# Kernel optimization log

Measured on AMD Instinct MI355X. Metric: run time of the kernel, lower is better.

## Reference

```python
import jax, jax.numpy as jnp
import numpy as np

B, T, N, H, E, K, HOR, OD = 64, 12, 1024, 64, 16, 3, 12, 1
DIN = 1  # input_dim
EPS = 1e-12


def setup_inputs() -> dict:
    key = jax.random.key(0)
    ks = jax.random.split(key, 8)
    s = 0.02
    return {
        "source": jax.random.normal(ks[0], (B, T, N, DIN), jnp.float32),
        "node_emb": jax.random.normal(ks[1], (N, E), jnp.float32),
        "time_emb": jax.random.normal(ks[2], (T, E), jnp.float32),
        "gate_wp": jax.random.normal(ks[3], (E, K, DIN + H, 2 * H), jnp.float32) * s,
        "gate_bp": jax.random.normal(ks[4], (E, 2 * H), jnp.float32) * s,
        "gate_lng": jnp.ones((E,), jnp.float32),
        "gate_lnb": jnp.zeros((E,), jnp.float32),
        "upd_wp": jax.random.normal(ks[5], (E, K, DIN + H, H), jnp.float32) * s,
        "upd_bp": jax.random.normal(ks[6], (E, H), jnp.float32) * s,
        "upd_lng": jnp.ones((E,), jnp.float32),
        "upd_lnb": jnp.zeros((E,), jnp.float32),
        "out_lng": jnp.ones((H,), jnp.float32),
        "out_lnb": jnp.zeros((H,), jnp.float32),
        "conv_w": jax.random.normal(ks[7], (HOR * OD, H), jnp.float32) * s,
        "conv_b": jnp.zeros((HOR * OD,), jnp.float32),
    }


def _ln(x, g, b):
    m = x.mean(-1, keepdims=True)
    v = x.var(-1, keepdims=True)
    return (x - m) / jnp.sqrt(v + EPS) * g + b


def _dagcn(x, node_emb, t_emb, wp, bp, lng, lnb):
    # x: [B, N, C]; node_emb: [N, E]; t_emb: [E] (one timestep)
    e = _ln(node_emb + t_emb[None, :], lng, lnb)          # [N, E] (dropout off in eval)
    sup = jax.nn.softmax(e @ e.T, axis=1)                  # [N, N]
    sl = [jnp.eye(N, dtype=x.dtype), sup]
    for _ in range(2, K):
        sl.append(2.0 * sup @ sl[-1] - sl[-2])             # Chebyshev recursion
    S = jnp.stack(sl, axis=0)                              # [K, N, N]
    w = jnp.einsum('nd,dkio->nkio', e, wp)                 # per-node weights
    bias = e @ bp                                          # [N, O]
    xg = jnp.einsum('knm,bmc->bnkc', S, x)                 # graph conv
    return jnp.einsum('bnki,nkio->bno', xg, w) + bias


def reference(source, node_emb, time_emb, gate_wp, gate_bp, gate_lng, gate_lnb,
              upd_wp, upd_bp, upd_lng, upd_lnb, out_lng, out_lnb, conv_w, conv_b):
    def step(state, xs):
        x_t, te = xs                                        # [B,N,DIN], [E]
        zr = jax.nn.sigmoid(_dagcn(jnp.concatenate([x_t, state], -1),
                                   node_emb, te, gate_wp, gate_bp, gate_lng, gate_lnb))
        z, r = zr[..., :H], zr[..., H:]
        hc = jnp.tanh(_dagcn(jnp.concatenate([x_t, z * state], -1),
                             node_emb, te, upd_wp, upd_bp, upd_lng, upd_lnb))
        h = r * state + (1.0 - r) * hc
        return h, None

    xs = jnp.swapaxes(source, 0, 1)                        # [T,B,N,DIN]
    h0 = jnp.zeros((B, N, H), source.dtype)
    h, _ = jax.lax.scan(step, h0, (xs, time_emb))          # last hidden state [B,N,H]
    y = _ln(h, out_lng, out_lnb)                           # out_dropout off in eval
    out = jnp.einsum('bnh,oh->bon', y, conv_w) + conv_b[None, :, None]  # end_conv
    return out.reshape(B, HOR, OD, N).transpose(0, 1, 3, 2)  # [B,horizon,N,output_dim]
```

## Files before the change

### kernel.cpp

```cpp
#include <hip/hip_runtime.h>
#include <math.h>

namespace {
constexpr int B_ = 64, T_ = 12, N_ = 1024, H_ = 64, E_ = 16;
constexpr int C_  = 65;
constexpr int BC_ = B_ * C_;
constexpr int OG_ = 128;
constexpr int OU_ = 64;
constexpr float EPS_ = 1e-12f;
constexpr int NP_ = 4224;
constexpr int KP_ = 224;
constexpr int COLG_ = OG_ * KP_;
constexpr int COLU_ = OU_ * KP_;
constexpr int NE_ = N_ * E_;
}

typedef unsigned short u16;
typedef unsigned int u32;
using f16x8 = __attribute__((ext_vector_type(8))) _Float16;
using f16x4 = __attribute__((ext_vector_type(4))) _Float16;
using f32x4 = __attribute__((ext_vector_type(4))) float;

__device__ __forceinline__ u32 div65(u32 x) { return (x * 16135u) >> 20; }

__device__ __forceinline__ void gl_lds16(const void* g, void* l, int lane) {
#if __has_builtin(__builtin_amdgcn_global_load_lds)
  __builtin_amdgcn_global_load_lds((const __attribute__((address_space(1))) u32*)g,
                                   (__attribute__((address_space(3))) u32*)l, 16, 0, 0);
#else
  *(uint4*)((char*)l + lane * 16) = *(const uint4*)g;
#endif
}

__device__ __forceinline__ void wprep_body(const float* __restrict__ wp, int NO,
                                           _Float16* __restrict__ wpC, int k, int tid) {
  if (tid >= NO) return;
  f16x8 lo = {}, hi = {};
  if (k < 195) {
    const u32 seg = div65((u32)k);
    const u32 ii = k - seg * 65;
#pragma unroll
    for (int d = 0; d < 8; d++)
      lo[d] = (_Float16)wp[(((size_t)d * 3 + seg) * 65 + ii) * NO + tid];
#pragma unroll
    for (int d = 0; d < 8; d++)
      hi[d] = (_Float16)wp[(((size_t)(d + 8) * 3 + seg) * 65 + ii) * NO + tid];
  }
  _Float16* dst = &wpC[((size_t)tid * KP_ + k) * 16];
  *(f16x8*)dst = lo;
  *(f16x8*)(dst + 8) = hi;
}

__device__ __forceinline__ void sup_body(const float* __restrict__ eT,
                                         _Float16* __restrict__ s16,
                                         int n, int tid, float* red) {
  float en[E_];
#pragma unroll
  for (int d = 0; d < E_; d++) en[d] = eT[d * N_ + n];
  float lg[4];
  float mx = -3.4e38f;
#pragma unroll
  for (int j = 0; j < 4; j++) {
    int m = tid + 256 * j;
    float s = 0.f;
#pragma unroll
    for (int d = 0; d < E_; d++) s = fmaf(en[d], eT[d * N_ + m], s);
    lg[j] = s;
    mx = fmaxf(mx, s);
  }
  red[tid] = mx; __syncthreads();
  for (int off = 128; off > 0; off >>= 1) {
    if (tid < off) red[tid] = fmaxf(red[tid], red[tid + off]);
    __syncthreads();
  }
  mx = red[0]; __syncthreads();
  float sum = 0.f;
#pragma unroll
  for (int j = 0; j < 4; j++) { lg[j] = __expf(lg[j] - mx); sum += lg[j]; }
  red[tid] = sum; __syncthreads();
  for (int off = 128; off > 0; off >>= 1) {
    if (tid < off) red[tid] += red[tid + off];
    __syncthreads();
  }
  float inv = 1.0f / red[0];
#pragma unroll
  for (int j = 0; j < 4; j++)
    s16[(size_t)n * N_ + tid + 256 * j] = (_Float16)(lg[j] * inv);
}

__device__ __forceinline__ void wgen_body(const float* __restrict__ e,
                                          const _Float16* __restrict__ wpC, int COLS,
                                          _Float16* __restrict__ Wt,
                                          int xb, int yb, int tid, float (*es)[16]) {
  const int col0 = xb * 1024 + tid * 4;
  const int n0 = yb * 64;
#pragma unroll
  for (int q = 0; q < 4; q++) {
    int idx = tid + q * 256;
    es[idx >> 4][idx & 15] = e[(size_t)n0 * 16 + idx];
  }
  __syncthreads();
  float wc[4][16];
#pragma unroll
  for (int cc = 0; cc < 4; cc++) {
    f16x8 a = *(const f16x8*)&wpC[(size_t)(col0 + cc) * 16];
    f16x8 b = *(const f16x8*)&wpC[(size_t)(col0 + cc) * 16 + 8];
#pragma unroll
    for (int d = 0; d < 8; d++) { wc[cc][d] = (float)a[d]; wc[cc][8 + d] = (float)b[d]; }
  }
  for (int nn = 0; nn < 64; nn++) {
    float acc[4] = {};
#pragma unroll
    for (int d = 0; d < 16; d++) {
      float ev = es[nn][d];
#pragma unroll
      for (int cc = 0; cc < 4; cc++) acc[cc] = fmaf(ev, wc[cc][d], acc[cc]);
    }
    f16x4 pv;
#pragma unroll
    for (int cc = 0; cc < 4; cc++) pv[cc] = (_Float16)acc[cc];
    *(f16x4*)&Wt[(size_t)(n0 + nn) * COLS + col0] = pv;
  }
}

__device__ __forceinline__ void gemm_body(
    const _Float16* __restrict__ A, const _Float16* __restrict__ Bt,
    _Float16* __restrict__ yt, _Float16* xg, int segoff, int combine,
    int bx, int by, int tid, _Float16* As, _Float16* Bs) {
  const int wave = tid >> 6, lane = tid & 63;
  const int m0 = by * 128, c0 = bx * 64;
  const int lrow = lane >> 3;
  const int lchunk = lane & 7;
  const int fm = lane & 15, fq = lane >> 4;
  f32x4 acc[2][4] = {};
  for (int ks = 0; ks < 16; ks++) {
    const int kp = ks * 64;
#pragma unroll
    for (int q = 0; q < 4; q++) {
      const int seg = wave * 4 + q;
      const int row = seg * 8 + lrow;
      const int sw = lchunk ^ (row & 7);
      gl_lds16(A + (size_t)(m0 + row) * 1024 + kp + sw * 8, &As[seg * 8 * 64], lane);
    }
#pragma unroll
    for (int q = 0; q < 2; q++) {
      const int seg = wave * 2 + q;
      const int row = seg * 8 + lrow;
      const int sw = lchunk ^ (row & 7);
      gl_lds16(Bt + (size_t)(c0 + row) * 1024 + kp + sw * 8, &Bs[seg * 8 * 64], lane);
    }
    __syncthreads();
#pragma unroll
    for (int kk = 0; kk < 2; kk++) {
      f16x8 af[2], bfr[4];
      const int g = kk * 4 + fq;
#pragma unroll
      for (int mt = 0; mt < 2; mt++) {
        const int row = wave * 32 + mt * 16 + fm;
        af[mt] = *(const f16x8*)&As[row * 64 + (g ^ (row & 7)) * 8];
      }
#pragma unroll
      for (int nt = 0; nt < 4; nt++) {
        const int row = nt * 16 + fm;
        bfr[nt] = *(const f16x8*)&Bs[row * 64 + (g ^ (row & 7)) * 8];
      }
#pragma unroll
      for (int mt = 0; mt < 2; mt++)
#pragma unroll
        for (int nt = 0; nt < 4; nt++)
          acc[mt][nt] = __builtin_amdgcn_mfma_f32_16x16x32_f16(af[mt], bfr[nt], acc[mt][nt], 0, 0, 0);
    }
    __syncthreads();
  }
  const int q4 = fq * 4;
#pragma unroll
  for (int nt = 0; nt < 4; nt++) {
    const int col = c0 + nt * 16 + fm;
    if (col >= BC_) continue;
    const u32 bq = div65((u32)col), cq = (u32)col - bq * 65;
#pragma unroll
    for (int mt = 0; mt < 2; mt++) {
      const int row = m0 + wave * 32 + mt * 16 + q4;
      const f32x4 v = acc[mt][nt];
      if (yt) {
        f16x4 pv;
#pragma unroll
        for (int j = 0; j < 4; j++) pv[j] = (_Float16)v[j];
        *(f16x4*)&yt[(size_t)col * 1024 + row] = pv;
      }
#pragma unroll
      for (int j = 0; j < 4; j++) {
        size_t base = ((size_t)(row + j) * 64 + bq) * KP_;
        float vv = v[j];
        if (combine) vv = 2.f * vv - (float)xg[base + cq];
        xg[base + segoff + cq] = (_Float16)vv;
      }
    }
  }
}

__global__ __launch_bounds__(256) void k_pre0(
    const float* __restrict__ gate_wp, const float* __restrict__ upd_wp,
    _Float16* __restrict__ wpCg, _Float16* __restrict__ wpCu,
    const float* __restrict__ node_emb, const float* __restrict__ time_emb,
    const float* __restrict__ g_lng, const float* __restrict__ g_lnb,
    const float* __restrict__ u_lng, const float* __restrict__ u_lnb,
    float* __restrict__ eg_all, float* __restrict__ egT_all,
    float* __restrict__ eu_all, float* __restrict__ euT_all) {
  const int bid = blockIdx.x, tid = threadIdx.x;
  if (bid < KP_)     { wprep_body(gate_wp, OG_, wpCg, bid, tid); return; }
  if (bid < 2 * KP_) { wprep_body(upd_wp,  OU_, wpCu, bid - KP_, tid); return; }
  const int idx = bid - 2 * KP_;
  const int t = idx >> 2;
  const int n = (idx & 3) * 256 + tid;
  float v[E_];
  float m = 0.f;
#pragma unroll
  for (int d = 0; d < E_; d++) { v[d] = node_emb[n * E_ + d] + time_emb[t * E_ + d]; m += v[d]; }
  m *= (1.0f / E_);
  float var = 0.f;
#pragma unroll
  for (int d = 0; d < E_; d++) { float x = v[d] - m; var += x * x; }
  var *= (1.0f / E_);
  float rs = rsqrtf(var + EPS_);
#pragma unroll
  for (int d = 0; d < E_; d++) {
    float nv = (v[d] - m) * rs;
    float g = nv * g_lng[d] + g_lnb[d];
    float u = nv * u_lng[d] + u_lnb[d];
    eg_all[(size_t)t * NE_ + n * E_ + d] = g;
    egT_all[(size_t)t * NE_ + d * N_ + n] = g;
    eu_all[(size_t)t * NE_ + n * E_ + d] = u;
    euT_all[(size_t)t * NE_ + d * N_ + n] = u;
  }
}

__global__ __launch_bounds__(256) void k_pro(
    const float* __restrict__ egT0, const float* __restrict__ euT0,
    const float* __restrict__ src,
    _Float16* __restrict__ supG, _Float16* __restrict__ supU0,
    _Float16* __restrict__ Xt, _Float16* __restrict__ xg) {
  __shared__ float red[256];
  const int bid = blockIdx.x, tid = threadIdx.x;
  if (bid < 1024) { sup_body(egT0, supG, bid, tid, red); return; }
  if (bid < 2048) { sup_body(euT0, supU0, bid - 1024, tid, red); return; }
  const int idx = bid - 2048;
  const int b = idx & 63, m0 = (idx >> 6) * 64;
  for (int q = 0; q < 17; q++) {
    int i = tid + q * 256;
    if (i < 64 * 65) {
      int c = i >> 6, m = i & 63;
      float xv = (c == 0) ? src[((size_t)b * T_) * N_ + m0 + m] : 0.f;
      Xt[((size_t)(b * C_ + c)) * 1024 + m0 + m] = (_Float16)xv;
      u32 mm = div65((u32)i), cc = (u32)i - mm * 65;
      float xv2 = (cc == 0) ? src[((size_t)b * T_) * N_ + m0 + mm] : 0.f;
      xg[((size_t)(m0 + mm) * 64 + b) * KP_ + cc] = (_Float16)xv2;
    }
  }
#pragma unroll
  for (int q = 0; q < 8; q++) {
    int i = tid + q * 256;
    int mm = i >> 5, kk = 192 + (i & 31);
    xg[((size_t)(m0 + mm) * 64 + b) * KP_ + kk] = (_Float16)0.f;
  }
}

__global__ __launch_bounds__(256) void k_tr(const _Float16* __restrict__ xg,
                                            _Float16* __restrict__ Xt) {
  __shared__ _Float16 tile[64][66];
  const int b = blockIdx.x & 63, m0 = (blockIdx.x >> 6) * 64;
  const int tid = threadIdx.x;
  {
    const int m = tid >> 2, c4 = tid & 3;
    const _Float16* rp = &xg[((size_t)(m0 + m) * 64 + b) * KP_ + c4 * 16];
    f16x8 v0 = *(const f16x8*)rp;
    f16x8 v1 = *(const f16x8*)(rp + 8);
#pragma unroll
    for (int i = 0; i < 8; i++) {
      tile[m][c4 * 16 + i] = v0[i];
      tile[m][c4 * 16 + 8 + i] = v1[i];
    }
    if (c4 == 0) tile[m][64] = rp[64];
  }
  __syncthreads();
  {
    const int m = tid & 63, cg = tid >> 6;
    for (int cc = cg; cc < 65; cc += 4)
      Xt[((size_t)(b * C_ + cc)) * 1024 + m0 + m] = tile[m][cc];
  }
}

__global__ __launch_bounds__(256) void k_g1(
    const _Float16* __restrict__ supG, const _Float16* __restrict__ Xt,
    _Float16* __restrict__ y1t, _Float16* xg,
    const float* __restrict__ eg_t, const _Float16* __restrict__ wpCg,
    _Float16* __restrict__ WtG) {
  __shared__ __align__(16) _Float16 smem[12288];
  const int bid = blockIdx.x, tid = threadIdx.x;
  if (bid < 528) {
    gemm_body(supG, Xt, y1t, xg, 65, 0, bid % 66, bid / 66, tid, smem, smem + 8192);
  } else {
    const int w = bid - 528;
    wgen_body(eg_t, wpCg, COLG_, WtG, w % 28, w / 28, tid, (float(*)[16])smem);
  }
}

__global__ __launch_bounds__(256) void k_g2(
    const _Float16* __restrict__ supG, const _Float16* __restrict__ y1t,
    _Float16* xg) {
  __shared__ __align__(16) _Float16 smem[12288];
  gemm_body(supG, y1t, nullptr, xg, 130, 1, blockIdx.x % 66, blockIdx.x / 66,
            threadIdx.x, smem, smem + 8192);
}

__global__ __launch_bounds__(256) void k_g3(
    const _Float16* __restrict__ supU, const _Float16* __restrict__ Xt,
    _Float16* __restrict__ y1t, _Float16* xg,
    const float* __restrict__ eu_t, const _Float16* __restrict__ wpCu,
    _Float16* __restrict__ WtU) {
  __shared__ __align__(16) _Float16 smem[12288];
  const int bid = blockIdx.x, tid = threadIdx.x;
  if (bid < 528) {
    gemm_body(supU, Xt, y1t, xg, 65, 0, bid % 66, bid / 66, tid, smem, smem + 8192);
  } else {
    const int w = bid - 528;
    wgen_body(eu_t, wpCu, COLU_, WtU, w % 14, w / 14, tid, (float(*)[16])smem);
  }
}

__global__ __launch_bounds__(256) void k_g4(
    const _Float16* __restrict__ supU, const _Float16* __restrict__ y1t,
    _Float16* xg,
    const float* __restrict__ egT_nx, const float* __restrict__ euT_nx,
    _Float16* __restrict__ supG, _Float16* __restrict__ supU_nx, int dosup) {
  __shared__ __align__(16) _Float16 smem[12288];
  const int bid = blockIdx.x, tid = threadIdx.x;
  if (bid < 528) {
    gemm_body(supU, y1t, nullptr, xg, 130, 1, bid % 66, bid / 66, tid, smem, smem + 8192);
  } else if (dosup) {
    if (bid < 1552) sup_body(egT_nx, supG, bid - 528, tid, (float*)smem);
    else            sup_body(euT_nx, supU_nx, bid - 1552, tid, (float*)smem);
  }
}

__global__ __launch_bounds__(256) void k_cg(
    const float* __restrict__ eg, const _Float16* XG,
    const _Float16* __restrict__ Wt, const float* __restrict__ bp,
    const _Float16* __restrict__ h16, const float* __restrict__ src, int t,
    _Float16* __restrict__ r16, _Float16* xgo) {
  const int n = blockIdx.x;
  const int tid = threadIdx.x;
  const int wave = tid >> 6, lane = tid & 63;
  const int fm = lane & 15, fq = lane >> 4;
  const int wm = wave >> 1, wn = wave & 1;
  __shared__ float es[16];
  __shared__ float bias_s[128];
  __shared__ _Float16 zs[64][72];
  __shared__ _Float16 rs[64][72];
  if (tid < 16) es[tid] = eg[n * 16 + tid];
  __syncthreads();
  if (tid < 128) {
    float bv = 0.f;
#pragma unroll
    for (int d = 0; d < 16; d++) bv = fmaf(es[d], bp[d * OG_ + tid], bv);
    bias_s[tid] = bv;
  }
  const _Float16* Ab = XG + (size_t)n * 64 * KP_;
  const _Float16* Bb = Wt + (size_t)n * OG_ * KP_;
  f16x8 af[2][2], bf[2][4];
#pragma unroll
  for (int mt = 0; mt < 2; mt++)
    af[0][mt] = *(const f16x8*)&Ab[(wm * 32 + mt * 16 + fm) * KP_ + fq * 8];
#pragma unroll
  for (int nt = 0; nt < 4; nt++)
    bf[0][nt] = *(const f16x8*)&Bb[(wn * 64 + nt * 16 + fm) * KP_ + fq * 8];
  f32x4 acc[2][4] = {};
#pragma unroll
  for (int kk = 0; kk < 7; kk++) {
    const int cur = kk & 1;
    if (kk < 6) {
      const int ko = (kk + 1) * 32 + fq * 8;
#pragma unroll
      for (int mt = 0; mt < 2; mt++)
        af[cur ^ 1][mt] = *(const f16x8*)&Ab[(wm * 32 + mt * 16 + fm) * KP_ + ko];
#pragma unroll
      for (int nt = 0; nt < 4; nt++)
        bf[cur ^ 1][nt] = *(const f16x8*)&Bb[(wn * 64 + nt * 16 + fm) * KP_ + ko];
    }
#pragma unroll
    for (int mt = 0; mt < 2; mt++)
#pragma unroll
      for (int nt = 0; nt < 4; nt++)
        acc[mt][nt] = __builtin_amdgcn_mfma_f32_16x16x32_f16(af[cur][mt], bf[cur][nt], acc[mt][nt], 0, 0, 0);
  }
  __syncthreads();
#pragma unroll
  for (int nt = 0; nt < 4; nt++) {
    const int o = wn * 64 + nt * 16 + fm;
    const float bias = bias_s[o];
#pragma unroll
    for (int mt = 0; mt < 2; mt++) {
      const f32x4 v = acc[mt][nt];
#pragma unroll
      for (int j = 0; j < 4; j++) {
        const int b = wm * 32 + mt * 16 + fq * 4 + j;
        float s = 1.0f / (1.0f + __expf(-(v[j] + bias)));
        if (wn == 0) zs[b][o] = (_Float16)s;
        else         rs[b][o - H_] = (_Float16)s;
      }
    }
  }
  __syncthreads();
  {
    const int b = tid >> 2, q = tid & 3;
    const _Float16* hp = &h16[((size_t)b * N_ + n) * H_ + q * 16];
    _Float16* xp = &xgo[((size_t)n * 64 + b) * KP_ + 1 + q * 16];
    _Float16* rp = &r16[((size_t)b * N_ + n) * H_ + q * 16];
    f16x8 r0, r1;
#pragma unroll
    for (int i = 0; i < 8; i++) {
      r0[i] = rs[b][q * 16 + i];
      r1[i] = rs[b][q * 16 + 8 + i];
    }
    *(f16x8*)rp = r0;
    *(f16x8*)(rp + 8) = r1;
    f16x8 h0 = *(const f16x8*)hp;
    f16x8 h1 = *(const f16x8*)(hp + 8);
    f16x8 x0, x1;
#pragma unroll
    for (int i = 0; i < 8; i++) {
      x0[i] = (_Float16)((float)zs[b][q * 16 + i] * (float)h0[i]);
      x1[i] = (_Float16)((float)zs[b][q * 16 + 8 + i] * (float)h1[i]);
    }
    *(f16x8*)xp = x0;
    *(f16x8*)(xp + 8) = x1;
    if (tid < 64) {
      float sv = src[((size_t)tid * T_ + t) * N_ + n];
      xgo[((size_t)n * 64 + tid) * KP_] = (_Float16)sv;
    }
  }
}

__global__ __launch_bounds__(256) void k_cu(
    const float* __restrict__ eu, const _Float16* XG,
    const _Float16* __restrict__ Wt, const float* __restrict__ bp,
    const _Float16* __restrict__ r16, const float* __restrict__ src,
    int t, int donext,
    _Float16* __restrict__ h16, _Float16* xgo) {
  const int n = blockIdx.x;
  const int tid = threadIdx.x;
  const int wave = tid >> 6, lane = tid & 63;
  const int fm = lane & 15, fq = lane >> 4;
  __shared__ float es[16];
  __shared__ float bias_s[64];
  __shared__ _Float16 hs[64][72];
  __shared__ _Float16 rs[64][72];
  if (tid < 16) es[tid] = eu[n * 16 + tid];
  __syncthreads();
  if (tid < 64) {
    float bv = 0.f;
#pragma unroll
    for (int d = 0; d < 16; d++) bv = fmaf(es[d], bp[d * OU_ + tid], bv);
    bias_s[tid] = bv;
  }
  {
    const int b = tid >> 2, q = tid & 3;
    const _Float16* hp = &h16[((size_t)b * N_ + n) * H_ + q * 16];
    const _Float16* rp = &r16[((size_t)b * N_ + n) * H_ + q * 16];
    f16x8 h0 = *(const f16x8*)hp;
    f16x8 h1 = *(const f16x8*)(hp + 8);
    f16x8 r0 = *(const f16x8*)rp;
    f16x8 r1 = *(const f16x8*)(rp + 8);
#pragma unroll
    for (int i = 0; i < 8; i++) {
      hs[b][q * 16 + i] = h0[i];
      hs[b][q * 16 + 8 + i] = h1[i];
      rs[b][q * 16 + i] = r0[i];
      rs[b][q * 16 + 8 + i] = r1[i];
    }
  }
  __syncthreads();
  const _Float16* Ab = XG + (size_t)n * 64 * KP_;
  const _Float16* Bb = Wt + (size_t)n * OU_ * KP_;
  f16x8 af[2], bf[2][4];
  af[0] = *(const f16x8*)&Ab[(wave * 16 + fm) * KP_ + fq * 8];
#pragma unroll
  for (int nt = 0; nt < 4; nt++)
    bf[0][nt] = *(const f16x8*)&Bb[(nt * 16 + fm) * KP_ + fq * 8];
  f32x4 acc[4] = {};
#pragma unroll
  for (int kk = 0; kk < 7; kk++) {
    const int cur = kk & 1;
    if (kk < 6) {
      const int ko = (kk + 1) * 32 + fq * 8;
      af[cur ^ 1] = *(const f16x8*)&Ab[(wave * 16 + fm) * KP_ + ko];
#pragma unroll
      for (int nt = 0; nt < 4; nt++)
        bf[cur ^ 1][nt] = *(const f16x8*)&Bb[(nt * 16 + fm) * KP_ + ko];
    }
#pragma unroll
    for (int nt = 0; nt < 4; nt++)
      acc[nt] = __builtin_amdgcn_mfma_f32_16x16x32_f16(af[cur], bf[cur][nt], acc[nt], 0, 0, 0);
  }
#pragma unroll
  for (int nt = 0; nt < 4; nt++) {
    const int o = nt * 16 + fm;
    const float bias = bias_s[o];
    const f32x4 v = acc[nt];
#pragma unroll
    for (int j = 0; j < 4; j++) {
      const int b = wave * 16 + fq * 4 + j;
      float hc = tanhf(v[j] + bias);
      float rv = (float)rs[b][o];
      float hv = (float)hs[b][o];
      hs[b][o] = (_Float16)(rv * hv + (1.0f - rv) * hc);
    }
  }
  __syncthreads();
  {
    const int b = tid >> 2, q = tid & 3;
    _Float16* hp = &h16[((size_t)b * N_ + n) * H_ + q * 16];
    f16x8 h0, h1;
#pragma unroll
    for (int i = 0; i < 8; i++) {
      h0[i] = hs[b][q * 16 + i];
      h1[i] = hs[b][q * 16 + 8 + i];
    }
    *(f16x8*)hp = h0;
    *(f16x8*)(hp + 8) = h1;
    if (donext) {
      _Float16* xp = &xgo[((size_t)n * 64 + b) * KP_ + 1 + q * 16];
      *(f16x8*)xp = h0;
      *(f16x8*)(xp + 8) = h1;
      if (tid < 64) {
        float sv = src[((size_t)tid * T_ + (t + 1)) * N_ + n];
        xgo[((size_t)n * 64 + tid) * KP_] = (_Float16)sv;
      }
    }
  }
}

__global__ __launch_bounds__(256) void k_final(const _Float16* __restrict__ h16,
                                               const float* __restrict__ out_lng,
                                               const float* __restrict__ out_lnb,
                                               const float* __restrict__ conv_w,
                                               const float* __restrict__ conv_b,
                                               float* __restrict__ out) {
  const int b = blockIdx.x >> 2;
  const int n = (blockIdx.x & 3) * 256 + threadIdx.x;
  __shared__ float cw[12][64];
  __shared__ float cb[12];
  __shared__ float lgs[64], lbs[64];
  for (int idx = threadIdx.x; idx < 12 * 64; idx += 256) cw[idx >> 6][idx & 63] = conv_w[idx];
  if (threadIdx.x < 12) cb[threadIdx.x] = conv_b[threadIdx.x];
  if (threadIdx.x < 64) { lgs[threadIdx.x] = out_lng[threadIdx.x]; lbs[threadIdx.x] = out_lnb[threadIdx.x]; }
  __syncthreads();
  const _Float16* hp = &h16[((size_t)b * N_ + n) * H_];
  float hv[64];
  float mean = 0.f;
#pragma unroll
  for (int i8 = 0; i8 < 8; i8++) {
    f16x8 v = *(const f16x8*)&hp[i8 * 8];
#pragma unroll
    for (int j = 0; j < 8; j++) { hv[i8 * 8 + j] = (float)v[j]; mean += hv[i8 * 8 + j]; }
  }
  mean *= (1.0f / H_);
  float var = 0.f;
#pragma unroll
  for (int i = 0; i < 64; i++) { float d = hv[i] - mean; var += d * d; }
  var *= (1.0f / H_);
  const float rs = rsqrtf(var + EPS_);
  float y[64];
#pragma unroll
  for (int i = 0; i < 64; i++)
    y[i] = (hv[i] - mean) * rs * lgs[i] + lbs[i];
#pragma unroll
  for (int o = 0; o < 12; o++) {
    float acc = cb[o];
#pragma unroll
    for (int i = 0; i < 64; i++) acc = fmaf(y[i], cw[o][i], acc);
    out[((size_t)b * 12 + o) * N_ + n] = acc;
  }
}

extern "C" void kernel_launch(void* const* d_in, const int* in_sizes, int n_in,
                              void* d_out, int out_size, void* d_ws, size_t ws_size,
                              hipStream_t stream) {
  const float* src      = (const float*)d_in[0];
  const float* node_emb = (const float*)d_in[1];
  const float* time_emb = (const float*)d_in[2];
  const float* gate_wp  = (const float*)d_in[3];
  const float* gate_bp  = (const float*)d_in[4];
  const float* gate_lng = (const float*)d_in[5];
  const float* gate_lnb = (const float*)d_in[6];
  const float* upd_wp   = (const float*)d_in[7];
  const float* upd_bp   = (const float*)d_in[8];
  const float* upd_lng  = (const float*)d_in[9];
  const float* upd_lnb  = (const float*)d_in[10];
  const float* out_lng  = (const float*)d_in[11];
  const float* out_lnb  = (const float*)d_in[12];
  const float* conv_w   = (const float*)d_in[13];
  const float* conv_b   = (const float*)d_in[14];
  float* out = (float*)d_out;

  constexpr size_t SZ_H16 = (size_t)B_ * N_ * H_ / 2;
  constexpr size_t SZ_R   = SZ_H16;
  constexpr size_t SZ_T   = (size_t)NP_ * 1024 / 2;
  constexpr size_t SZ_XG  = (size_t)N_ * 64 * KP_ / 2;
  constexpr size_t SZ_WT  = (size_t)N_ * OG_ * KP_ / 2;
  constexpr size_t SZ_WCG = (size_t)COLG_ * 16 / 2;
  constexpr size_t SZ_WCU = (size_t)COLU_ * 16 / 2;
  constexpr size_t SZ_S   = (size_t)N_ * N_ / 2;

  float* ws = (float*)d_ws;
  size_t off = 0;
  float* h16F   = ws + off; off += SZ_H16;
  float* r16F   = ws + off; off += SZ_R;
  float* XtF    = ws + off; off += SZ_T;
  float* y1tF   = ws + off; off += SZ_T;
  float* xgF    = ws + off; off += SZ_XG;
  float* WtF    = ws + off; off += SZ_WT;
  float* wcgF   = ws + off; off += SZ_WCG;
  float* wcuF   = ws + off; off += SZ_WCU;
  float* supGF  = ws + off; off += SZ_S;
  float* supUF  = ws + off; off += 2 * SZ_S;
  float* eg_all  = ws + off; off += (size_t)T_ * NE_;
  float* egT_all = ws + off; off += (size_t)T_ * NE_;
  float* eu_all  = ws + off; off += (size_t)T_ * NE_;
  float* euT_all = ws + off; off += (size_t)T_ * NE_;
  if (ws_size < off * sizeof(float)) return;

  _Float16* h16  = (_Float16*)h16F;
  _Float16* r16  = (_Float16*)r16F;
  _Float16* Xt   = (_Float16*)XtF;
  _Float16* y1t  = (_Float16*)y1tF;
  _Float16* xg   = (_Float16*)xgF;
  _Float16* WtG  = (_Float16*)WtF;
  _Float16* WtU  = (_Float16*)WtF;
  _Float16* wpCg = (_Float16*)wcgF;
  _Float16* wpCu = (_Float16*)wcuF;
  _Float16* supG = (_Float16*)supGF;
  _Float16* supU = (_Float16*)supUF;

  hipMemsetAsync(h16, 0, SZ_H16 * sizeof(float), stream);
  k_pre0<<<2 * KP_ + 48, 256, 0, stream>>>(gate_wp, upd_wp, wpCg, wpCu,
                                           node_emb, time_emb,
                                           gate_lng, gate_lnb, upd_lng, upd_lnb,
                                           eg_all, egT_all, eu_all, euT_all);
  k_pro<<<3072, 256, 0, stream>>>(egT_all, euT_all, src, supG, supU, Xt, xg);

  for (int t = 0; t < T_; t++) {
    _Float16* sU  = supU + (size_t)(t & 1) * N_ * N_;
    _Float16* sUn = supU + (size_t)((t + 1) & 1) * N_ * N_;
    const float* eg_t = eg_all + (size_t)t * NE_;
    const float* eu_t = eu_all + (size_t)t * NE_;
    const int tn = (t < T_ - 1) ? t + 1 : t;
    const int more = (t < T_ - 1) ? 1 : 0;
    k_g1<<<976, 256, 0, stream>>>(supG, Xt, y1t, xg, eg_t, wpCg, WtG);
    k_g2<<<528, 256, 0, stream>>>(supG, y1t, xg);
    k_cg<<<N_, 256, 0, stream>>>(eg_t, xg, WtG, gate_bp, h16, src, t, r16, xg);
    k_tr<<<1024, 256, 0, stream>>>(xg, Xt);
    k_g3<<<752, 256, 0, stream>>>(sU, Xt, y1t, xg, eu_t, wpCu, WtU);
    k_g4<<<2576, 256, 0, stream>>>(sU, y1t, xg,
                                   egT_all + (size_t)tn * NE_,
                                   euT_all + (size_t)tn * NE_,
                                   supG, sUn, more);
    k_cu<<<N_, 256, 0, stream>>>(eu_t, xg, WtU, upd_bp, r16, src, t, more, h16, xg);
    if (more) k_tr<<<1024, 256, 0, stream>>>(xg, Xt);
  }
  k_final<<<B_ * N_ / 256, 256, 0, stream>>>(h16, out_lng, out_lnb, conv_w, conv_b, out);
}
```

Measured before the change: 2.067 ms.

## Precompute squared support matrix to remove dependent second graph-conv GEMM

Instead of computing S·X and then S·(S·X) in two dependent launches, the Chebyshev term is rewritten as (S·S)·X so both graph-conv GEMMs run in a single launch. S² for the next timestep is computed ahead of time: S is transposed via LDS tiles and S·Sᵀ-style GEMMs run alongside the current step's work. This removes two kernel launches and their serialization per step, but adds an N×N×N GEMM per support matrix per step, extra transpose passes, and more workspace for double-buffered supports and squares. S² is rounded to fp16 before use, which slightly changes numerics.

Measured after the change: 1.971 ms. 1.05x faster.

```diff
diff --git a/kernel.cpp b/kernel.cpp
--- a/kernel.cpp
+++ b/kernel.cpp
@@ -8,7 +8,6 @@
 constexpr int OG_ = 128;
 constexpr int OU_ = 64;
 constexpr float EPS_ = 1e-12f;
-constexpr int NP_ = 4224;
 constexpr int KP_ = 224;
 constexpr int COLG_ = OG_ * KP_;
 constexpr int COLU_ = OU_ * KP_;
@@ -123,9 +122,34 @@
   }
 }
 
+__device__ __forceinline__ void supT_body(const _Float16* __restrict__ S,
+                                          _Float16* __restrict__ ST,
+                                          int tile, int tid, _Float16 (*lds)[66]) {
+  const int n0 = (tile >> 4) * 64;
+  const int m0 = (tile & 15) * 64;
+  {
+    const int r = tid >> 2, c0 = (tid & 3) * 16;
+    const _Float16* sp = &S[(size_t)(n0 + r) * 1024 + m0 + c0];
+    f16x8 a = *(const f16x8*)sp;
+    f16x8 b = *(const f16x8*)(sp + 8);
+#pragma unroll
+    for (int i = 0; i < 8; i++) { lds[r][c0 + i] = a[i]; lds[r][c0 + 8 + i] = b[i]; }
+  }
+  __syncthreads();
+  {
+    const int c = tid >> 2, r0 = (tid & 3) * 16;
+    f16x8 a, b;
+#pragma unroll
+    for (int i = 0; i < 8; i++) { a[i] = lds[r0 + i][c]; b[i] = lds[r0 + 8 + i][c]; }
+    _Float16* dp = &ST[(size_t)(m0 + c) * 1024 + n0 + r0];
+    *(f16x8*)dp = a;
+    *(f16x8*)(dp + 8) = b;
+  }
+}
+
 __device__ __forceinline__ void gemm_body(
     const _Float16* __restrict__ A, const _Float16* __restrict__ Bt,
-    _Float16* __restrict__ yt, _Float16* xg, int segoff, int combine,
+    _Float16* xg, int segoff, int combine, _Float16* __restrict__ rowout,
     int bx, int by, int tid, _Float16* As, _Float16* Bs) {
   const int wave = tid >> 6, lane = tid & 63;
   const int m0 = by * 128, c0 = bx * 64;
@@ -176,18 +200,23 @@
 #pragma unroll
   for (int nt = 0; nt < 4; nt++) {
     const int col = c0 + nt * 16 + fm;
+    if (rowout) {
+#pragma unroll
+      for (int mt = 0; mt < 2; mt++) {
+        const int row = m0 + wave * 32 + mt * 16 + q4;
+        const f32x4 v = acc[mt][nt];
+#pragma unroll
+        for (int j = 0; j < 4; j++)
+          rowout[(size_t)(row + j) * 1024 + col] = (_Float16)v[j];
+      }
+      continue;
+    }
     if (col >= BC_) continue;
     const u32 bq = div65((u32)col), cq = (u32)col - bq * 65;
 #pragma unroll
     for (int mt = 0; mt < 2; mt++) {
       const int row = m0 + wave * 32 + mt * 16 + q4;
       const f32x4 v = acc[mt][nt];
-      if (yt) {
-        f16x4 pv;
-#pragma unroll
-        for (int j = 0; j < 4; j++) pv[j] = (_Float16)v[j];
-        *(f16x4*)&yt[(size_t)col * 1024 + row] = pv;
-      }
 #pragma unroll
       for (int j = 0; j < 4; j++) {
         size_t base = ((size_t)(row + j) * 64 + bq) * KP_;
@@ -265,6 +294,27 @@
   }
 }
 
+__global__ __launch_bounds__(256) void k_proT(
+    const _Float16* __restrict__ supG0, const _Float16* __restrict__ supU0,
+    _Float16* __restrict__ supGT, _Float16* __restrict__ supUT) {
+  __shared__ _Float16 lds[64][66];
+  const int bid = blockIdx.x;
+  if (bid < 256) supT_body(supG0, supGT, bid, threadIdx.x, lds);
+  else           supT_body(supU0, supUT, bid - 256, threadIdx.x, lds);
+}
+
+__global__ __launch_bounds__(256) void k_pro2(
+    const _Float16* __restrict__ supG0, const _Float16* __restrict__ supGT,
+    const _Float16* __restrict__ supU0, const _Float16* __restrict__ supUT,
+    _Float16* __restrict__ sup2G0, _Float16* __restrict__ sup2U0) {
+  __shared__ __align__(16) _Float16 smem[12288];
+  const int bid = blockIdx.x, tid = threadIdx.x;
+  if (bid < 128)
+    gemm_body(supG0, supGT, nullptr, 0, 0, sup2G0, bid % 16, bid / 16, tid, smem, smem + 8192);
+  else
+    gemm_body(supU0, supUT, nullptr, 0, 0, sup2U0, (bid - 128) % 16, (bid - 128) / 16, tid, smem, smem + 8192);
+}
+
 __global__ __launch_bounds__(256) void k_tr(const _Float16* __restrict__ xg,
                                             _Float16* __restrict__ Xt) {
   __shared__ _Float16 tile[64][66];
@@ -290,73 +340,54 @@
   }
 }
 
-__global__ __launch_bounds__(256) void k_g1(
-    const _Float16* __restrict__ supG, const _Float16* __restrict__ Xt,
-    _Float16* __restrict__ y1t, _Float16* xg,
+__global__ __launch_bounds__(256) void k_ga(
+    const _Float16* __restrict__ supG_t, const _Float16* __restrict__ sup2G_t,
+    const _Float16* __restrict__ Xt, _Float16* xg,
     const float* __restrict__ eg_t, const _Float16* __restrict__ wpCg,
-    _Float16* __restrict__ WtG) {
+    _Float16* __restrict__ WtG,
+    const float* __restrict__ egT_nx, const float* __restrict__ euT_nx,
+    _Float16* __restrict__ supG_nx, _Float16* __restrict__ supU_nx) {
   __shared__ __align__(16) _Float16 smem[12288];
   const int bid = blockIdx.x, tid = threadIdx.x;
   if (bid < 528) {
-    gemm_body(supG, Xt, y1t, xg, 65, 0, bid % 66, bid / 66, tid, smem, smem + 8192);
+    gemm_body(supG_t, Xt, xg, 65, 0, nullptr, bid % 66, bid / 66, tid, smem, smem + 8192);
+  } else if (bid < 1056) {
+    const int w = bid - 528;
+    gemm_body(sup2G_t, Xt, xg, 130, 1, nullptr, w % 66, w / 66, tid, smem, smem + 8192);
+  } else if (bid < 1504) {
+    const int w = bid - 1056;
+    wgen_body(eg_t, wpCg, COLG_, WtG, w % 28, w / 28, tid, (float(*)[16])smem);
+  } else if (bid < 2528) {
+    sup_body(egT_nx, supG_nx, bid - 1504, tid, (float*)smem);
   } else {
-    const int w = bid - 528;
-    wgen_body(eg_t, wpCg, COLG_, WtG, w % 28, w / 28, tid, (float(*)[16])smem);
-  }
-}
-
-__global__ __launch_bounds__(256) void k_g2(
-    const _Float16* __restrict__ supG, const _Float16* __restrict__ y1t,
-    _Float16* xg) {
-  __shared__ __align__(16) _Float16 smem[12288];
-  gemm_body(supG, y1t, nullptr, xg, 130, 1, blockIdx.x % 66, blockIdx.x / 66,
-            threadIdx.x, smem, smem + 8192);
-}
-
-__global__ __launch_bounds__(256) void k_g3(
-    const _Float16* __restrict__ supU, const _Float16* __restrict__ Xt,
-    _Float16* __restrict__ y1t, _Float16* xg,
-    const float* __restrict__ eu_t, const _Float16* __restrict__ wpCu,
-    _Float16* __restrict__ WtU) {
-  __shared__ __align__(16) _Float16 smem[12288];
-  const int bid = blockIdx.x, tid = threadIdx.x;
-  if (bid < 528) {
-    gemm_body(supU, Xt, y1t, xg, 65, 0, bid % 66, bid / 66, tid, smem, smem + 8192);
-  } else {
-    const int w = bid - 528;
-    wgen_body(eu_t, wpCu, COLU_, WtU, w % 14, w / 14, tid, (float(*)[16])smem);
-  }
-}
-
-__global__ __launch_bounds__(256) void k_g4(
-    const _Float16* __restrict__ supU, const _Float16* __restrict__ y1t,
-    _Float16* xg,
-    const float* __restrict__ egT_nx, const float* __restrict__ euT_nx,
-    _Float16* __restrict__ supG, _Float16* __restrict__ supU_nx, int dosup) {
-  __shared__ __align__(16) _Float16 smem[12288];
-  const int bid = blockIdx.x, tid = threadIdx.x;
-  if (bid < 528) {
-    gemm_body(supU, y1t, nullptr, xg, 130, 1, bid % 66, bid / 66, tid, smem, smem + 8192);
-  } else if (dosup) {
-    if (bid < 1552) sup_body(egT_nx, supG, bid - 528, tid, (float*)smem);
-    else            sup_body(euT_nx, supU_nx, bid - 1552, tid, (float*)smem);
-  }
-}
-
-__global__ __launch_bounds__(256) void k_cg(
+    sup_body(euT_nx, supU_nx, bid - 2528, tid, (float*)smem);
+  }
+}
+
+__global__ __launch_bounds__(256) void k_cgT(
     const float* __restrict__ eg, const _Float16* XG,
     const _Float16* __restrict__ Wt, const float* __restrict__ bp,
     const _Float16* __restrict__ h16, const float* __restrict__ src, int t,
-    _Float16* __restrict__ r16, _Float16* xgo) {
-  const int n = blockIdx.x;
+    _Float16* __restrict__ r16, _Float16* xgo,
+    const _Float16* __restrict__ supG_nx, const _Float16* __restrict__ supU_nx,
+    _Float16* __restrict__ supGT, _Float16* __restrict__ supUT) {
+  __shared__ __align__(16) char smraw[19456];
+  const int bid = blockIdx.x;
   const int tid = threadIdx.x;
+  if (bid >= 1024) {
+    _Float16 (*lds)[66] = (_Float16(*)[66])smraw;
+    if (bid < 1280) supT_body(supG_nx, supGT, bid - 1024, tid, lds);
+    else            supT_body(supU_nx, supUT, bid - 1280, tid, lds);
+    return;
+  }
+  float* es = (float*)smraw;
+  float* bias_s = (float*)(smraw + 64);
+  _Float16 (*zs)[72] = (_Float16(*)[72])(smraw + 576);
+  _Float16 (*rs)[72] = (_Float16(*)[72])(smraw + 9792);
+  const int n = bid;
   const int wave = tid >> 6, lane = tid & 63;
   const int fm = lane & 15, fq = lane >> 4;
   const int wm = wave >> 1, wn = wave & 1;
-  __shared__ float es[16];
-  __shared__ float bias_s[128];
-  __shared__ _Float16 zs[64][72];
-  __shared__ _Float16 rs[64][72];
   if (tid < 16) es[tid] = eg[n * 16 + tid];
   __syncthreads();
   if (tid < 128) {
@@ -438,6 +469,33 @@
       float sv = src[((size_t)tid * T_ + t) * N_ + n];
       xgo[((size_t)n * 64 + tid) * KP_] = (_Float16)sv;
     }
+  }
+}
+
+__global__ __launch_bounds__(256) void k_gu(
+    const _Float16* __restrict__ supU_t, const _Float16* __restrict__ sup2U_t,
+    const _Float16* __restrict__ Xt, _Float16* xg,
+    const float* __restrict__ eu_t, const _Float16* __restrict__ wpCu,
+    _Float16* __restrict__ WtU,
+    const _Float16* __restrict__ supG_nx, const _Float16* __restrict__ supGT,
+    const _Float16* __restrict__ supU_nx, const _Float16* __restrict__ supUT,
+    _Float16* __restrict__ sup2G_nx, _Float16* __restrict__ sup2U_nx) {
+  __shared__ __align__(16) _Float16 smem[12288];
+  const int bid = blockIdx.x, tid = threadIdx.x;
+  if (bid < 528) {
+    gemm_body(supU_t, Xt, xg, 65, 0, nullptr, bid % 66, bid / 66, tid, smem, smem + 8192);
+  } else if (bid < 1056) {
+    const int w = bid - 528;
+    gemm_body(sup2U_t, Xt, xg, 130, 1, nullptr, w % 66, w / 66, tid, smem, smem + 8192);
+  } else if (bid < 1280) {
+    const int w = bid - 1056;
+    wgen_body(eu_t, wpCu, COLU_, WtU, w % 14, w / 14, tid, (float(*)[16])smem);
+  } else if (bid < 1408) {
+    const int w = bid - 1280;
+    gemm_body(supG_nx, supGT, nullptr, 0, 0, sup2G_nx, w % 16, w / 16, tid, smem, smem + 8192);
+  } else {
+    const int w = bid - 1408;
+    gemm_body(supU_nx, supUT, nullptr, 0, 0, sup2U_nx, w % 16, w / 16, tid, smem, smem + 8192);
   }
 }
 
@@ -605,7 +663,7 @@
 
   constexpr size_t SZ_H16 = (size_t)B_ * N_ * H_ / 2;
   constexpr size_t SZ_R   = SZ_H16;
-  constexpr size_t SZ_T   = (size_t)NP_ * 1024 / 2;
+  constexpr size_t SZ_T   = (size_t)BC_ * 1024 / 2;
   constexpr size_t SZ_XG  = (size_t)N_ * 64 * KP_ / 2;
   constexpr size_t SZ_WT  = (size_t)N_ * OG_ * KP_ / 2;
   constexpr size_t SZ_WCG = (size_t)COLG_ * 16 / 2;
@@ -617,30 +675,37 @@
   float* h16F   = ws + off; off += SZ_H16;
   float* r16F   = ws + off; off += SZ_R;
   float* XtF    = ws + off; off += SZ_T;
-  float* y1tF   = ws + off; off += SZ_T;
   float* xgF    = ws + off; off += SZ_XG;
   float* WtF    = ws + off; off += SZ_WT;
   float* wcgF   = ws + off; off += SZ_WCG;
   float* wcuF   = ws + off; off += SZ_WCU;
-  float* supGF  = ws + off; off += SZ_S;
+  float* supGF  = ws + off; off += 2 * SZ_S;
   float* supUF  = ws + off; off += 2 * SZ_S;
+  float* supGTF = ws + off; off += SZ_S;
+  float* supUTF = ws + off; off += SZ_S;
+  float* s2GF   = ws + off; off += 2 * SZ_S;
+  float* s2UF   = ws + off; off += 2 * SZ_S;
   float* eg_all  = ws + off; off += (size_t)T_ * NE_;
   float* egT_all = ws + off; off += (size_t)T_ * NE_;
   float* eu_all  = ws + off; off += (size_t)T_ * NE_;
   float* euT_all = ws + off; off += (size_t)T_ * NE_;
   if (ws_size < off * sizeof(float)) return;
 
-  _Float16* h16  = (_Float16*)h16F;
-  _Float16* r16  = (_Float16*)r16F;
-  _Float16* Xt   = (_Float16*)XtF;
-  _Float16* y1t  = (_Float16*)y1tF;
-  _Float16* xg   = (_Float16*)xgF;
-  _Float16* WtG  = (_Float16*)WtF;
-  _Float16* WtU  = (_Float16*)WtF;
-  _Float16* wpCg = (_Float16*)wcgF;
-  _Float16* wpCu = (_Float16*)wcuF;
-  _Float16* supG = (_Float16*)supGF;
-  _Float16* supU = (_Float16*)supUF;
+  _Float16* h16   = (_Float16*)h16F;
+  _Float16* r16   = (_Float16*)r16F;
+  _Float16* Xt    = (_Float16*)XtF;
+  _Float16* xg    = (_Float16*)xgF;
+  _Float16* WtG   = (_Float16*)WtF;
+  _Float16* WtU   = (_Float16*)WtF;
+  _Float16* wpCg  = (_Float16*)wcgF;
+  _Float16* wpCu  = (_Float16*)wcuF;
+  _Float16* supG  = (_Float16*)supGF;
+  _Float16* supU  = (_Float16*)supUF;
+  _Float16* supGT = (_Float16*)supGTF;
+  _Float16* supUT = (_Float16*)supUTF;
+  _Float16* s2G   = (_Float16*)s2GF;
+  _Float16* s2U   = (_Float16*)s2UF;
+  const size_t SB = (size_t)N_ * N_;
 
   hipMemsetAsync(h16, 0, SZ_H16 * sizeof(float), stream);
   k_pre0<<<2 * KP_ + 48, 256, 0, stream>>>(gate_wp, upd_wp, wpCg, wpCu,
@@ -648,23 +713,34 @@
                                            gate_lng, gate_lnb, upd_lng, upd_lnb,
                                            eg_all, egT_all, eu_all, euT_all);
   k_pro<<<3072, 256, 0, stream>>>(egT_all, euT_all, src, supG, supU, Xt, xg);
+  k_proT<<<512, 256, 0, stream>>>(supG, supU, supGT, supUT);
+  k_pro2<<<256, 256, 0, stream>>>(supG, supGT, supU, supUT, s2G, s2U);
 
   for (int t = 0; t < T_; t++) {
-    _Float16* sU  = supU + (size_t)(t & 1) * N_ * N_;
-    _Float16* sUn = supU + (size_t)((t + 1) & 1) * N_ * N_;
+    const int cur = t & 1, nxt = (t + 1) & 1;
+    _Float16* supG_t  = supG + (size_t)cur * SB;
+    _Float16* supG_nx = supG + (size_t)nxt * SB;
+    _Float16* supU_t  = supU + (size_t)cur * SB;
+    _Float16* supU_nx = supU + (size_t)nxt * SB;
+    _Float16* s2G_t   = s2G + (size_t)cur * SB;
+    _Float16* s2G_nx  = s2G + (size_t)nxt * SB;
+    _Float16* s2U_t   = s2U + (size_t)cur * SB;
+    _Float16* s2U_nx  = s2U + (size_t)nxt * SB;
     const float* eg_t = eg_all + (size_t)t * NE_;
     const float* eu_t = eu_all + (size_t)t * NE_;
-    const int tn = (t < T_ - 1) ? t + 1 : t;
     const int more = (t < T_ - 1) ? 1 : 0;
-    k_g1<<<976, 256, 0, stream>>>(supG, Xt, y1t, xg, eg_t, wpCg, WtG);
-    k_g2<<<528, 256, 0, stream>>>(supG, y1t, xg);
-    k_cg<<<N_, 256, 0, stream>>>(eg_t, xg, WtG, gate_bp, h16, src, t, r16, xg);
+    const int tn = more ? t + 1 : t;
+
+    k_ga<<<more ? 3552 : 1504, 256, 0, stream>>>(
+        supG_t, s2G_t, Xt, xg, eg_t, wpCg, WtG,
+        egT_all + (size_t)tn * NE_, euT_all + (size_t)tn * NE_, supG_nx, supU_nx);
+    k_cgT<<<more ? 1536 : 1024, 256, 0, stream>>>(
+        eg_t, xg, WtG, gate_bp, h16, src, t, r16, xg,
+        supG_nx, supU_nx, supGT, supUT);
     k_tr<<<1024, 256, 0, stream>>>(xg, Xt);
-    k_g3<<<752, 256, 0, stream>>>(sU, Xt, y1t, xg, eu_t, wpCu, WtU);
-    k_g4<<<2576, 256, 0, stream>>>(sU, y1t, xg,
-                                   egT_all + (size_t)tn * NE_,
-                                   euT_all + (size_t)tn * NE_,
-                                   supG, sUn, more);
+    k_gu<<<more ? 1536 : 1280, 256, 0, stream>>>(
+        supU_t, s2U_t, Xt, xg, eu_t, wpCu, WtU,
+        supG_nx, supGT, supU_nx, supUT, s2G_nx, s2U_nx);
     k_cu<<<N_, 256, 0, stream>>>(eu_t, xg, WtU, upd_bp, r16, src, t, more, h16, xg);
     if (more) k_tr<<<1024, 256, 0, stream>>>(xg, Xt);
   }
```
